# Kernel optimization log

Measured on AMD Instinct MI355X. Metric: run time of the kernel, lower is better.

The kernel has to match this reference:

```python
import jax, jax.numpy as jnp
import numpy as np

H = 768          # hidden_size
HH = H // 2      # 384


def setup_inputs() -> dict:
    key = jax.random.key(0)
    ks = jax.random.split(key, 16)
    B, W, E, R = 32, 512, 128, 1024
    inp = {
        "hidden_states": jax.random.normal(ks[0], (B, W, H), dtype=jnp.float32),
        "relation_head": jax.random.randint(ks[1], (B, R), 0, E),
        "relation_tail": jax.random.randint(ks[2], (B, R), 0, E),
        "relation_label": jax.random.randint(ks[3], (B, R), 0, 2),
        "entities_start": jax.random.randint(ks[4], (B, E), 0, W),
        "entities_end": jax.random.randint(ks[5], (B, E), 0, W),
        "entities_label": jax.random.randint(ks[6], (B, E), 0, 3),
        # parameters (torch Linear convention: weight [out, in])
        "entity_emb": jax.random.normal(ks[7], (3, H), dtype=jnp.float32) * 0.02,
        "Wh1": jax.random.normal(ks[8], (H, 2 * H), dtype=jnp.float32) * 0.02,
        "bh1": jnp.zeros((H,), jnp.float32),
        "Wh2": jax.random.normal(ks[9], (HH, H), dtype=jnp.float32) * 0.02,
        "bh2": jnp.zeros((HH,), jnp.float32),
        "Wt1": jax.random.normal(ks[10], (H, 2 * H), dtype=jnp.float32) * 0.02,
        "bt1": jnp.zeros((H,), jnp.float32),
        "Wt2": jax.random.normal(ks[11], (HH, H), dtype=jnp.float32) * 0.02,
        "bt2": jnp.zeros((HH,), jnp.float32),
        "W_bil": jax.random.normal(ks[12], (2, HH, HH), dtype=jnp.float32) * 0.02,
        "W_lin": jax.random.normal(ks[13], (2, 2 * HH), dtype=jnp.float32) * 0.02,
        "b_lin": jnp.zeros((2,), jnp.float32),
    }
    return inp


def _ffnn(x, W1, b1, W2, b2):
    # two-layer MLP with ReLU (dropout is identity in eval mode)
    h = jax.nn.relu(jnp.einsum('brd,hd->brh', x, W1) + b1)
    return jax.nn.relu(jnp.einsum('brh,oh->bro', h, W2) + b2)


def reference(hidden_states, relation_head, relation_tail, relation_label,
              entities_start, entities_end, entities_label,
              entity_emb, Wh1, bh1, Wh2, bh2, Wt1, bt1, Wt2, bt2,
              W_bil, W_lin, b_lin):
    # gather per-relation entity info: [B, R]
    head_index = jnp.take_along_axis(entities_start, relation_head, axis=1)
    head_label = jnp.take_along_axis(entities_label, relation_head, axis=1)
    tail_index = jnp.take_along_axis(entities_start, relation_tail, axis=1)
    tail_label = jnp.take_along_axis(entities_label, relation_tail, axis=1)

    # gather token reprs: [B, R, H]
    head_tok = jnp.take_along_axis(hidden_states, head_index[:, :, None], axis=1)
    tail_tok = jnp.take_along_axis(hidden_states, tail_index[:, :, None], axis=1)

    head_repr = jnp.concatenate([head_tok, entity_emb[head_label]], axis=-1)  # [B,R,2H]
    tail_repr = jnp.concatenate([tail_tok, entity_emb[tail_label]], axis=-1)

    heads = _ffnn(head_repr, Wh1, bh1, Wh2, bh2)  # [B,R,HH]
    tails = _ffnn(tail_repr, Wt1, bt1, Wt2, bt2)

    # biaffine: bilinear + linear on concat
    bil = jnp.einsum('bri,oij,brj->bro', heads, W_bil, tails)
    lin = jnp.einsum('brc,oc->bro', jnp.concatenate([heads, tails], axis=-1), W_lin) + b_lin
    logits = bil + lin  # [B, R, 2]

    # per-doc mean CE summed over docs
    logp = jax.nn.log_softmax(logits, axis=-1)
    nll = -jnp.take_along_axis(logp, relation_label[:, :, None], axis=-1)[..., 0]  # [B,R]
    loss = jnp.sum(jnp.mean(nll, axis=1))
    return loss
```

## Files before the change

kernel.cpp:

```cpp
#include <hip/hip_runtime.h>
#include <math.h>

typedef unsigned short u16;
typedef __bf16 bf16x8 __attribute__((ext_vector_type(8)));
typedef float f32x4 __attribute__((ext_vector_type(4)));

#define B_ 32
#define W_ 512
#define H_ 768
#define HH_ 384
#define E_ 128
#define R_ 1024
#define BE_ (B_*E_)
#define K1_ (2*H_)

__device__ __forceinline__ u16 f2bf(float f) {
  unsigned u = __float_as_uint(f);
  u = (u + 0x7fffu + ((u >> 16) & 1u)) >> 16;
  return (u16)u;
}
__device__ __forceinline__ float bf2f(u16 u) {
  return __uint_as_float(((unsigned)u) << 16);
}

__device__ __forceinline__ void gload_lds16(const void* g, void* l) {
  __builtin_amdgcn_global_load_lds(
      (__attribute__((address_space(1))) void*)(g),
      (__attribute__((address_space(3))) void*)(l), 16, 0, 0);
}

__device__ __forceinline__ void xcd_swizzle(int& bx, int& by) {
  const int nwg = gridDim.x * gridDim.y;
  int orig = blockIdx.y * gridDim.x + blockIdx.x;
  int q = nwg >> 3, r = nwg & 7;
  int xcd = orig & 7, idx = orig >> 3;
  int wgid = (xcd < r ? xcd * (q + 1) : r * (q + 1) + (xcd - r) * q) + idx;
  bx = wgid % gridDim.x;
  by = wgid / gridDim.x;
}

#define NBLK_W 2017
#define NBLK_P 1152
#define NBLK_X 4096

__global__ __launch_bounds__(256) void prep_all(
    const float* __restrict__ Wh1, const float* __restrict__ Wt1,
    const float* __restrict__ Wh2, const float* __restrict__ Wt2,
    const float* __restrict__ Wbil,
    const float* __restrict__ bh1, const float* __restrict__ bt1,
    const float* __restrict__ bh2, const float* __restrict__ bt2,
    const float* __restrict__ emb,
    const float* __restrict__ hs, const int* __restrict__ ent_start,
    u16* __restrict__ W1c, u16* __restrict__ W2c, u16* __restrict__ Wb,
    float* __restrict__ b2cat, float* __restrict__ P, u16* __restrict__ X)
{
  const int blk = blockIdx.x;
  const int tid = threadIdx.x;

  if (blk < NBLK_W) {
    const int i = blk * 256 + tid;
    const int SW1 = 294912;
    const int SW2 = SW1 + 147456;
    const int SWB = SW2 + 73728;
    const int SB2 = SWB + 192;
    if (i < SW1) {
      int row = i / 192, c = i % 192;
      const float4* src = (const float4*)((row < 768)
          ? (Wh1 + (size_t)row * K1_) : (Wt1 + (size_t)(row - 768) * K1_));
      float4 v = src[c];
      ushort4 o; o.x = f2bf(v.x); o.y = f2bf(v.y); o.z = f2bf(v.z); o.w = f2bf(v.w);
      ((ushort4*)W1c)[i] = o;
    } else if (i < SW2) {
      int j = i - SW1;
      float4 v = (j < 73728) ? ((const float4*)Wh2)[j]
                             : ((const float4*)Wt2)[j - 73728];
      ushort4 o; o.x = f2bf(v.x); o.y = f2bf(v.y); o.z = f2bf(v.z); o.w = f2bf(v.w);
      ((ushort4*)W2c)[j] = o;
    } else if (i < SWB) {
      int j = i - SW2;
      float4 v = ((const float4*)Wbil)[j];
      ushort4 o; o.x = f2bf(v.x); o.y = f2bf(v.y); o.z = f2bf(v.z); o.w = f2bf(v.w);
      ((ushort4*)Wb)[j] = o;
    } else if (i < SB2) {
      int j = i - SWB;
      ((float4*)b2cat)[j] = (j < 96) ? ((const float4*)bh2)[j]
                                     : ((const float4*)bt2)[j - 96];
    }
  } else if (blk < NBLK_W + NBLK_P) {
    const int w = (blk - NBLK_W) * 4 + (tid >> 6);
    const int lane = tid & 63;
    const int l = w / K1_;
    const int n = w - l * K1_;
    const float* wrow = (n < 768) ? (Wh1 + (size_t)n * K1_ + 768)
                                  : (Wt1 + (size_t)(n - 768) * K1_ + 768);
    const float  bb   = (n < 768) ? bh1[n] : bt1[n - 768];
    const float* ev = emb + (size_t)l * H_;
    float s = 0.f;
#pragma unroll
    for (int t = 0; t < 12; ++t) {
      int d = lane + 64 * t;
      s += ev[d] * wrow[d];
    }
#pragma unroll
    for (int off = 32; off; off >>= 1) s += __shfl_down(s, off);
    if (lane == 0) P[(size_t)l * K1_ + n] = s + bb;
  } else {
    const int be = blk - (NBLK_W + NBLK_P);
    if (tid < 192) {
      int b = be >> 7;
      int start = ent_start[be];
      const float4* s0 = (const float4*)(hs + ((size_t)b * W_ + start) * H_);
      float4 v = s0[tid];
      ushort4 o; o.x = f2bf(v.x); o.y = f2bf(v.y); o.z = f2bf(v.z); o.w = f2bf(v.w);
      ((ushort4*)(X + (size_t)be * H_))[tid] = o;
    }
  }
}

#define BM 128
#define BN 128
#define BKK 64

__global__ __launch_bounds__(256, 2) void gemm_bf16(
    const u16* __restrict__ A, int lda,
    const u16* __restrict__ Wt,
    const float* __restrict__ bias,
    u16* __restrict__ C, int ldc,
    int M, int N, int K, int do_relu, int half_n, int aoff,
    const float* __restrict__ rowBias,
    const int* __restrict__ rowLabel, int ldP)
{
  __shared__ char smem[2 * 32768];

  int bx, by;
  xcd_swizzle(bx, by);
  const int bn = bx * BN;
  const int bm = by * BM;

  const int tid  = threadIdx.x;
  const int wid  = tid >> 6;
  const int lane = tid & 63;
  const int wm = ((wid >> 1) & 1) * 64;
  const int wn = (wid & 1) * 64;

  const int a0 = (half_n && bn >= half_n) ? aoff : 0;

  const int srow = lane >> 3;
  const int sk8  = (lane & 7) ^ srow;
  const u16* gA = A  + (size_t)(bm + 32*wid + srow) * lda + a0 + 8*sk8;
  const u16* gB = Wt + (size_t)(bn + 32*wid + srow) * K  + 8*sk8;

  const int frow = lane & 15;
  const int fk8  = lane >> 4;

  f32x4 acc[4][4] = {};

  auto stage = [&](int buf, int k0) {
    char* As = smem + buf * 32768;
    char* Bs = As + 16384;
#pragma unroll
    for (int i = 0; i < 4; ++i) {
      gload_lds16(gA + k0 + (size_t)i * 8 * lda, As + (4*wid + i) * 1024);
      gload_lds16(gB + k0 + (size_t)i * 8 * K,   Bs + (4*wid + i) * 1024);
    }
  };

  const int nt = K / BKK;
  stage(0, 0);
  asm volatile("s_waitcnt vmcnt(0)" ::: "memory");
  __syncthreads();

  for (int t = 0; t < nt; ++t) {
    const int cur = t & 1;
    if (t + 1 < nt) stage(cur ^ 1, (t + 1) * BKK);

    char* As = smem + cur * 32768;
    char* Bs = As + 16384;
#pragma unroll
    for (int kh = 0; kh < 2; ++kh) {
      bf16x8 a[4], b[4];
#pragma unroll
      for (int m = 0; m < 4; ++m) {
        const int row  = wm + m*16 + frow;
        const int slot = (kh*4 + fk8) ^ (row & 7);
        a[m] = *(const bf16x8*)(As + row*128 + slot*16);
      }
#pragma unroll
      for (int n = 0; n < 4; ++n) {
        const int row  = wn + n*16 + frow;
        const int slot = (kh*4 + fk8) ^ (row & 7);
        b[n] = *(const bf16x8*)(Bs + row*128 + slot*16);
      }
#pragma unroll
      for (int m = 0; m < 4; ++m)
#pragma unroll
        for (int n = 0; n < 4; ++n)
          acc[m][n] = __builtin_amdgcn_mfma_f32_16x16x32_bf16(
              a[m], b[n], acc[m][n], 0, 0, 0);
    }

    if (t + 1 < nt) {
      asm volatile("s_waitcnt vmcnt(0)" ::: "memory");
      __syncthreads();
    }
  }

  int lbl[4][4];
  if (rowLabel) {
#pragma unroll
    for (int m = 0; m < 4; ++m)
#pragma unroll
      for (int r = 0; r < 4; ++r)
        lbl[m][r] = rowLabel[bm + wm + m*16 + fk8*4 + r];
  }

#pragma unroll
  for (int n = 0; n < 4; ++n) {
    const int col = bn + wn + n*16 + frow;
    const float bv = bias ? bias[col] : 0.f;
    float p0 = 0.f, p1 = 0.f, p2 = 0.f;
    if (rowLabel) {
      p0 = rowBias[col];
      p1 = rowBias[ldP + col];
      p2 = rowBias[2*ldP + col];
    }
#pragma unroll
    for (int m = 0; m < 4; ++m) {
#pragma unroll
      for (int r = 0; r < 4; ++r) {
        const int row = bm + wm + m*16 + fk8*4 + r;
        float v = acc[m][n][r] + bv;
        if (rowLabel) {
          int l = lbl[m][r];
          v += (l == 0) ? p0 : ((l == 1) ? p1 : p2);
        }
        if (do_relu) v = fmaxf(v, 0.f);
        C[(size_t)row * ldc + col] = f2bf(v);
      }
    }
  }
}

__global__ __launch_bounds__(256, 2) void gemm_S(
    const u16* __restrict__ Hcat, const u16* __restrict__ U,
    const float* __restrict__ linHT, const float* __restrict__ b_lin,
    float* __restrict__ S)
{
  __shared__ char smem[2 * 16384];

  int bx, by;
  xcd_swizzle(bx, by);
  const int z  = by >> 1;
  const int bm = (by & 1) * 64;
  const int bn = bx * 64;

  const int tid  = threadIdx.x;
  const int wid  = tid >> 6;
  const int lane = tid & 63;
  const int wm = ((wid >> 1) & 1) * 32;
  const int wn = (wid & 1) * 32;

  const int srow = lane >> 3;
  const int sk8  = (lane & 7) ^ srow;
  const u16* gA = Hcat + (size_t)z * 98304 + (size_t)(bm + 16*wid + srow) * 768 + 8*sk8;
  const u16* gB = U    + (size_t)z * 98304 + (size_t)(bn + 16*wid + srow) * 384 + 8*sk8;

  const int frow = lane & 15;
  const int fk8  = lane >> 4;

  f32x4 acc[2][2] = {};

  auto stage = [&](int buf, int k0) {
    char* As = smem + buf * 16384;
    char* Bs = As + 8192;
#pragma unroll
    for (int i = 0; i < 2; ++i) {
      gload_lds16(gA + k0 + (size_t)i * 8 * 768, As + (2*wid + i) * 1024);
      gload_lds16(gB + k0 + (size_t)i * 8 * 384, Bs + (2*wid + i) * 1024);
    }
  };

  const int nt = 384 / BKK;
  stage(0, 0);
  asm volatile("s_waitcnt vmcnt(0)" ::: "memory");
  __syncthreads();

  for (int t = 0; t < nt; ++t) {
    const int cur = t & 1;
    if (t + 1 < nt) stage(cur ^ 1, (t + 1) * BKK);

    char* As = smem + cur * 16384;
    char* Bs = As + 8192;
#pragma unroll
    for (int kh = 0; kh < 2; ++kh) {
      bf16x8 a[2], b[2];
#pragma unroll
      for (int m = 0; m < 2; ++m) {
        const int row  = wm + m*16 + frow;
        const int slot = (kh*4 + fk8) ^ (row & 7);
        a[m] = *(const bf16x8*)(As + row*128 + slot*16);
      }
#pragma unroll
      for (int n = 0; n < 2; ++n) {
        const int row  = wn + n*16 + frow;
        const int slot = (kh*4 + fk8) ^ (row & 7);
        b[n] = *(const bf16x8*)(Bs + row*128 + slot*16);
      }
#pragma unroll
      for (int m = 0; m < 2; ++m)
#pragma unroll
        for (int n = 0; n < 2; ++n)
          acc[m][n] = __builtin_amdgcn_mfma_f32_16x16x32_bf16(
              a[m], b[n], acc[m][n], 0, 0, 0);
    }

    if (t + 1 < nt) {
      asm volatile("s_waitcnt vmcnt(0)" ::: "memory");
      __syncthreads();
    }
  }

  const int o = frow & 1;
  const float blv = b_lin[o];
  float linH[2][4];
#pragma unroll
  for (int m = 0; m < 2; ++m)
#pragma unroll
    for (int r = 0; r < 4; ++r)
      linH[m][r] = linHT[(size_t)(z*128 + bm + wm + m*16 + fk8*4 + r) * 4 + o];

#pragma unroll
  for (int n = 0; n < 2; ++n) {
    const int n_out = bn + wn + n*16 + frow;
    const int e2 = n_out >> 1;
    const float lt = linHT[(size_t)(z*128 + e2) * 4 + 2 + o];
#pragma unroll
    for (int m = 0; m < 2; ++m) {
#pragma unroll
      for (int r = 0; r < 4; ++r) {
        const int row = bm + wm + m*16 + fk8*4 + r;
        S[((size_t)(z*128 + row)) * 256 + n_out] =
            acc[m][n][r] + linH[m][r] + lt + blv;
      }
    }
  }
}

__global__ __launch_bounds__(256) void lin_parts_kernel(
    const u16* __restrict__ Hcat, const float* __restrict__ W_lin,
    float* __restrict__ linHT, float* __restrict__ out)
{
  if (blockIdx.x == 0 && threadIdx.x == 0) out[0] = 0.f;
  const int wave = blockIdx.x * 4 + (threadIdx.x >> 6);
  const int lane = threadIdx.x & 63;
  const int nwave = gridDim.x * 4;

  for (int be = wave; be < BE_; be += nwave) {
    const ushort4* src = (const ushort4*)(Hcat + (size_t)be * 768);
    float s0 = 0.f, s1 = 0.f, s2 = 0.f, s3 = 0.f;
#pragma unroll
    for (int rd = 0; rd < 3; ++rd) {
      const int idx4 = rd * 64 + lane;
      const int c = idx4 * 4;
      ushort4 v4 = src[idx4];
      float4 w0 = *(const float4*)(W_lin + c);
      float4 w1 = *(const float4*)(W_lin + 768 + c);
      float d0 = bf2f(v4.x)*w0.x + bf2f(v4.y)*w0.y + bf2f(v4.z)*w0.z + bf2f(v4.w)*w0.w;
      float d1 = bf2f(v4.x)*w1.x + bf2f(v4.y)*w1.y + bf2f(v4.z)*w1.z + bf2f(v4.w)*w1.w;
      if (c < 384) { s0 += d0; s1 += d1; }
      else         { s2 += d0; s3 += d1; }
    }
#pragma unroll
    for (int off = 32; off; off >>= 1) {
      s0 += __shfl_down(s0, off);
      s1 += __shfl_down(s1, off);
      s2 += __shfl_down(s2, off);
      s3 += __shfl_down(s3, off);
    }
    if (lane == 0) {
      float4 v = {s0, s1, s2, s3};
      *(float4*)(linHT + (size_t)be * 4) = v;
    }
  }
}

__global__ __launch_bounds__(256) void ce_kernel(
    const int* __restrict__ rel_head, const int* __restrict__ rel_tail,
    const int* __restrict__ rel_label, const float* __restrict__ S,
    float* __restrict__ out)
{
  const int i = blockIdx.x * 256 + threadIdx.x;
  const int b  = i >> 10;
  const int rh = rel_head[i];
  const int rt = rel_tail[i];
  const int lab = rel_label[i];
  const float2 lv = *(const float2*)(S + ((size_t)(b*E_ + rh)) * 256 + rt*2);
  const float l0 = lv.x, l1 = lv.y;
  const float m = fmaxf(l0, l1);
  const float lse = m + logf(expf(l0 - m) + expf(l1 - m));
  float nll = lse - (lab == 0 ? l0 : l1);

#pragma unroll
  for (int off = 32; off; off >>= 1) nll += __shfl_down(nll, off);
  __shared__ float red[4];
  if ((threadIdx.x & 63) == 0) red[threadIdx.x >> 6] = nll;
  __syncthreads();
  if (threadIdx.x == 0)
    atomicAdd(out, (red[0] + red[1] + red[2] + red[3]) * (1.0f / R_));
}

extern "C" void kernel_launch(void* const* d_in, const int* in_sizes, int n_in,
                              void* d_out, int out_size, void* d_ws, size_t ws_size,
                              hipStream_t stream)
{
  const float* hs        = (const float*)d_in[0];
  const int*   rel_head  = (const int*)  d_in[1];
  const int*   rel_tail  = (const int*)  d_in[2];
  const int*   rel_label = (const int*)  d_in[3];
  const int*   ent_start = (const int*)  d_in[4];
  const int*   ent_label = (const int*)  d_in[6];
  const float* emb   = (const float*)d_in[7];
  const float* Wh1   = (const float*)d_in[8];
  const float* bh1   = (const float*)d_in[9];
  const float* Wh2   = (const float*)d_in[10];
  const float* bh2   = (const float*)d_in[11];
  const float* Wt1   = (const float*)d_in[12];
  const float* bt1   = (const float*)d_in[13];
  const float* Wt2   = (const float*)d_in[14];
  const float* bt2   = (const float*)d_in[15];
  const float* W_bil = (const float*)d_in[16];
  const float* W_lin = (const float*)d_in[17];
  const float* b_lin = (const float*)d_in[18];
  float* out = (float*)d_out;

  u16* X    = (u16*)d_ws;
  u16* H1   = X    + (size_t)BE_ * H_;
  u16* Hcat = H1   + (size_t)BE_ * K1_;
  u16* U    = Hcat + (size_t)BE_ * H_;
  u16* W1c  = U    + (size_t)BE_ * H_;
  u16* W2c  = W1c  + (size_t)K1_ * H_;
  u16* Wb   = W2c  + (size_t)H_ * H_;
  float* b2cat = (float*)(Wb + (size_t)H_ * HH_);
  float* P     = b2cat + H_;
  float* linHT = P + 3*K1_;
  float* S     = linHT + 4*BE_;

  prep_all<<<dim3(NBLK_W + NBLK_P + NBLK_X), dim3(256), 0, stream>>>(
      Wh1, Wt1, Wh2, Wt2, W_bil, bh1, bt1, bh2, bt2, emb,
      hs, ent_start, W1c, W2c, Wb, b2cat, P, X);

  gemm_bf16<<<dim3(K1_/BN, BE_/BM), dim3(256), 0, stream>>>(
      X, H_, W1c, (const float*)nullptr, H1, K1_, BE_, K1_, H_, 1, 0, 0,
      P, ent_label, K1_);

  gemm_bf16<<<dim3(H_/BN, BE_/BM), dim3(256), 0, stream>>>(
      H1, K1_, W2c, b2cat, Hcat, H_, BE_, H_, H_, 1, HH_, H_,
      (const float*)nullptr, (const int*)nullptr, 0);

  lin_parts_kernel<<<dim3(128), dim3(256), 0, stream>>>(Hcat, W_lin, linHT, out);

  gemm_bf16<<<dim3(H_/BN, BE_/BM), dim3(256), 0, stream>>>(
      Hcat + HH_, H_, Wb, (const float*)nullptr, U, H_, BE_, H_, HH_, 0, 0, 0,
      (const float*)nullptr, (const int*)nullptr, 0);

  gemm_S<<<dim3(4, 2*B_), dim3(256), 0, stream>>>(Hcat, U, linHT, b_lin, S);

  ce_kernel<<<dim3(B_*R_/256), dim3(256), 0, stream>>>(
      rel_head, rel_tail, rel_label, S, out);
}
```

Measured before the change: 68.35 us.

## Shrink GEMM tiles, fuse lin-parts into U GEMM, fuse CE into S GEMM

```diff
diff --git a/kernel.cpp b/kernel.cpp
--- a/kernel.cpp
+++ b/kernel.cpp
@@ -13,6 +13,7 @@
 #define R_ 1024
 #define BE_ (B_*E_)
 #define K1_ (2*H_)
+#define BKK 64
 
 __device__ __forceinline__ u16 f2bf(float f) {
   unsigned u = __float_as_uint(f);
@@ -27,16 +28,6 @@
   __builtin_amdgcn_global_load_lds(
       (__attribute__((address_space(1))) void*)(g),
       (__attribute__((address_space(3))) void*)(l), 16, 0, 0);
-}
-
-__device__ __forceinline__ void xcd_swizzle(int& bx, int& by) {
-  const int nwg = gridDim.x * gridDim.y;
-  int orig = blockIdx.y * gridDim.x + blockIdx.x;
-  int q = nwg >> 3, r = nwg & 7;
-  int xcd = orig & 7, idx = orig >> 3;
-  int wgid = (xcd < r ? xcd * (q + 1) : r * (q + 1) + (xcd - r) * q) + idx;
-  bx = wgid % gridDim.x;
-  by = wgid / gridDim.x;
 }
 
 #define NBLK_W 2017
@@ -117,53 +108,97 @@
   }
 }
 
-#define BM 128
-#define BN 128
-#define BKK 64
-
-__global__ __launch_bounds__(256, 2) void gemm_bf16(
+template<int TBM, int TBN, int MINB>
+__global__ __launch_bounds__(256, MINB) void gemm_t(
     const u16* __restrict__ A, int lda,
     const u16* __restrict__ Wt,
     const float* __restrict__ bias,
-    u16* __restrict__ C, int ldc,
-    int M, int N, int K, int do_relu, int half_n, int aoff,
+    u16* __restrict__ C, int ldc, int K,
+    int do_relu, int half_n, int aoff,
     const float* __restrict__ rowBias,
-    const int* __restrict__ rowLabel, int ldP)
+    const int* __restrict__ rowLabel, int ldP,
+    int nbx, int ngemm,
+    const u16* __restrict__ linSrc, const float* __restrict__ W_lin,
+    float* __restrict__ linHT, float* __restrict__ out)
 {
-  __shared__ char smem[2 * 32768];
-
-  int bx, by;
-  xcd_swizzle(bx, by);
-  const int bn = bx * BN;
-  const int bm = by * BM;
+  constexpr int FM = TBM / 32;
+  constexpr int FN = TBN / 32;
+  constexpr int UNITS = (TBM + TBN) / 8;
+  constexpr int UPW = UNITS / 4;
+  constexpr int BUFB = (TBM + TBN) * 128;
+
+  __shared__ char smem[2 * BUFB];
 
   const int tid  = threadIdx.x;
   const int wid  = tid >> 6;
   const int lane = tid & 63;
-  const int wm = ((wid >> 1) & 1) * 64;
-  const int wn = (wid & 1) * 64;
+
+  if ((int)blockIdx.x >= ngemm) {
+    if ((int)blockIdx.x == ngemm && tid == 0) out[0] = 0.f;
+    const int nblk  = gridDim.x - ngemm;
+    const int wave  = ((int)blockIdx.x - ngemm) * 4 + wid;
+    const int nwave = nblk * 4;
+    for (int be = wave; be < BE_; be += nwave) {
+      const ushort4* src = (const ushort4*)(linSrc + (size_t)be * 768);
+      float s0 = 0.f, s1 = 0.f, s2 = 0.f, s3 = 0.f;
+#pragma unroll
+      for (int rd = 0; rd < 3; ++rd) {
+        const int idx4 = rd * 64 + lane;
+        const int c = idx4 * 4;
+        ushort4 v4 = src[idx4];
+        float4 w0 = *(const float4*)(W_lin + c);
+        float4 w1 = *(const float4*)(W_lin + 768 + c);
+        float d0 = bf2f(v4.x)*w0.x + bf2f(v4.y)*w0.y + bf2f(v4.z)*w0.z + bf2f(v4.w)*w0.w;
+        float d1 = bf2f(v4.x)*w1.x + bf2f(v4.y)*w1.y + bf2f(v4.z)*w1.z + bf2f(v4.w)*w1.w;
+        if (c < 384) { s0 += d0; s1 += d1; }
+        else         { s2 += d0; s3 += d1; }
+      }
+#pragma unroll
+      for (int off = 32; off; off >>= 1) {
+        s0 += __shfl_down(s0, off);
+        s1 += __shfl_down(s1, off);
+        s2 += __shfl_down(s2, off);
+        s3 += __shfl_down(s3, off);
+      }
+      if (lane == 0) {
+        float4 v = {s0, s1, s2, s3};
+        *(float4*)(linHT + (size_t)be * 4) = v;
+      }
+    }
+    return;
+  }
+
+  const int q = ngemm >> 3, r = ngemm & 7;
+  const int xcd = blockIdx.x & 7, idx = blockIdx.x >> 3;
+  const int wgid = (xcd < r ? xcd * (q + 1) : r * (q + 1) + (xcd - r) * q) + idx;
+  const int bn = (wgid % nbx) * TBN;
+  const int bm = (wgid / nbx) * TBM;
 
   const int a0 = (half_n && bn >= half_n) ? aoff : 0;
-
   const int srow = lane >> 3;
   const int sk8  = (lane & 7) ^ srow;
-  const u16* gA = A  + (size_t)(bm + 32*wid + srow) * lda + a0 + 8*sk8;
-  const u16* gB = Wt + (size_t)(bn + 32*wid + srow) * K  + 8*sk8;
-
+
+  auto stage = [&](int buf, int k0) {
+    char* base = smem + buf * BUFB;
+#pragma unroll
+    for (int i = 0; i < UPW; ++i) {
+      const int u = wid * UPW + i;
+      if (u < TBM / 8) {
+        const int row = bm + u * 8 + srow;
+        gload_lds16(A + (size_t)row * lda + a0 + k0 + 8 * sk8, base + u * 1024);
+      } else {
+        const int row = bn + (u - TBM / 8) * 8 + srow;
+        gload_lds16(Wt + (size_t)row * K + k0 + 8 * sk8, base + u * 1024);
+      }
+    }
+  };
+
+  const int wm = (wid >> 1) * (TBM / 2);
+  const int wn = (wid & 1) * (TBN / 2);
   const int frow = lane & 15;
   const int fk8  = lane >> 4;
 
-  f32x4 acc[4][4] = {};
-
-  auto stage = [&](int buf, int k0) {
-    char* As = smem + buf * 32768;
-    char* Bs = As + 16384;
-#pragma unroll
-    for (int i = 0; i < 4; ++i) {
-      gload_lds16(gA + k0 + (size_t)i * 8 * lda, As + (4*wid + i) * 1024);
-      gload_lds16(gB + k0 + (size_t)i * 8 * K,   Bs + (4*wid + i) * 1024);
-    }
-  };
+  f32x4 acc[FM][FN] = {};
 
   const int nt = K / BKK;
   stage(0, 0);
@@ -174,27 +209,27 @@
     const int cur = t & 1;
     if (t + 1 < nt) stage(cur ^ 1, (t + 1) * BKK);
 
-    char* As = smem + cur * 32768;
-    char* Bs = As + 16384;
+    char* As = smem + cur * BUFB;
+    char* Bs = As + TBM * 128;
 #pragma unroll
     for (int kh = 0; kh < 2; ++kh) {
-      bf16x8 a[4], b[4];
-#pragma unroll
-      for (int m = 0; m < 4; ++m) {
+      bf16x8 a[FM], b[FN];
+#pragma unroll
+      for (int m = 0; m < FM; ++m) {
         const int row  = wm + m*16 + frow;
         const int slot = (kh*4 + fk8) ^ (row & 7);
         a[m] = *(const bf16x8*)(As + row*128 + slot*16);
       }
 #pragma unroll
-      for (int n = 0; n < 4; ++n) {
+      for (int n = 0; n < FN; ++n) {
         const int row  = wn + n*16 + frow;
         const int slot = (kh*4 + fk8) ^ (row & 7);
         b[n] = *(const bf16x8*)(Bs + row*128 + slot*16);
       }
 #pragma unroll
-      for (int m = 0; m < 4; ++m)
-#pragma unroll
-        for (int n = 0; n < 4; ++n)
+      for (int m = 0; m < FM; ++m)
+#pragma unroll
+        for (int n = 0; n < FN; ++n)
           acc[m][n] = __builtin_amdgcn_mfma_f32_16x16x32_bf16(
               a[m], b[n], acc[m][n], 0, 0, 0);
     }
@@ -205,17 +240,17 @@
     }
   }
 
-  int lbl[4][4];
+  int lbl[FM][4];
   if (rowLabel) {
 #pragma unroll
-    for (int m = 0; m < 4; ++m)
+    for (int m = 0; m < FM; ++m)
 #pragma unroll
       for (int r = 0; r < 4; ++r)
         lbl[m][r] = rowLabel[bm + wm + m*16 + fk8*4 + r];
   }
 
 #pragma unroll
-  for (int n = 0; n < 4; ++n) {
+  for (int n = 0; n < FN; ++n) {
     const int col = bn + wn + n*16 + frow;
     const float bv = bias ? bias[col] : 0.f;
     float p0 = 0.f, p1 = 0.f, p2 = 0.f;
@@ -225,7 +260,7 @@
       p2 = rowBias[2*ldP + col];
     }
 #pragma unroll
-    for (int m = 0; m < 4; ++m) {
+    for (int m = 0; m < FM; ++m) {
 #pragma unroll
       for (int r = 0; r < 4; ++r) {
         const int row = bm + wm + m*16 + fk8*4 + r;
@@ -241,53 +276,59 @@
   }
 }
 
-__global__ __launch_bounds__(256, 2) void gemm_S(
+__global__ __launch_bounds__(256, 2) void gemm_S_ce(
     const u16* __restrict__ Hcat, const u16* __restrict__ U,
     const float* __restrict__ linHT, const float* __restrict__ b_lin,
-    float* __restrict__ S)
+    const int* __restrict__ rel_head, const int* __restrict__ rel_tail,
+    const int* __restrict__ rel_label, float* __restrict__ out)
 {
   __shared__ char smem[2 * 16384];
-
-  int bx, by;
-  xcd_swizzle(bx, by);
-  const int z  = by >> 1;
-  const int bm = (by & 1) * 64;
-  const int bn = bx * 64;
+  __shared__ float Sl[64][65];
+  __shared__ float red[4];
+
+  const int xcd = blockIdx.x & 7, idx = blockIdx.x >> 3;
+  const int wgid = xcd * 32 + idx;
+  const int bn = (wgid & 3) * 64;
+  const int zz = wgid >> 2;
+  const int z  = zz >> 1;
+  const int bm = (zz & 1) * 64;
 
   const int tid  = threadIdx.x;
   const int wid  = tid >> 6;
   const int lane = tid & 63;
-  const int wm = ((wid >> 1) & 1) * 32;
-  const int wn = (wid & 1) * 32;
-
   const int srow = lane >> 3;
   const int sk8  = (lane & 7) ^ srow;
-  const u16* gA = Hcat + (size_t)z * 98304 + (size_t)(bm + 16*wid + srow) * 768 + 8*sk8;
-  const u16* gB = U    + (size_t)z * 98304 + (size_t)(bn + 16*wid + srow) * 384 + 8*sk8;
-
+
+  auto stage = [&](int buf, int k0) {
+    char* base = smem + buf * 16384;
+#pragma unroll
+    for (int i = 0; i < 4; ++i) {
+      const int u = wid * 4 + i;
+      if (u < 8) {
+        const int row = z*128 + bm + u*8 + srow;
+        gload_lds16(Hcat + (size_t)row * 768 + k0 + 8*sk8, base + u*1024);
+      } else {
+        const int row = bn + (u - 8)*8 + srow;
+        gload_lds16(U + (size_t)z*98304 + (size_t)row * 384 + k0 + 8*sk8,
+                    base + u*1024);
+      }
+    }
+  };
+
+  const int wm = (wid >> 1) * 32;
+  const int wn = (wid & 1) * 32;
   const int frow = lane & 15;
   const int fk8  = lane >> 4;
 
   f32x4 acc[2][2] = {};
 
-  auto stage = [&](int buf, int k0) {
-    char* As = smem + buf * 16384;
-    char* Bs = As + 8192;
-#pragma unroll
-    for (int i = 0; i < 2; ++i) {
-      gload_lds16(gA + k0 + (size_t)i * 8 * 768, As + (2*wid + i) * 1024);
-      gload_lds16(gB + k0 + (size_t)i * 8 * 384, Bs + (2*wid + i) * 1024);
-    }
-  };
-
-  const int nt = 384 / BKK;
   stage(0, 0);
   asm volatile("s_waitcnt vmcnt(0)" ::: "memory");
   __syncthreads();
 
-  for (int t = 0; t < nt; ++t) {
+  for (int t = 0; t < 6; ++t) {
     const int cur = t & 1;
-    if (t + 1 < nt) stage(cur ^ 1, (t + 1) * BKK);
+    if (t + 1 < 6) stage(cur ^ 1, (t + 1) * BKK);
 
     char* As = smem + cur * 16384;
     char* Bs = As + 8192;
@@ -314,98 +355,52 @@
               a[m], b[n], acc[m][n], 0, 0, 0);
     }
 
-    if (t + 1 < nt) {
+    if (t + 1 < 6) {
       asm volatile("s_waitcnt vmcnt(0)" ::: "memory");
       __syncthreads();
     }
   }
+  __syncthreads();
 
   const int o = frow & 1;
   const float blv = b_lin[o];
-  float linH[2][4];
-#pragma unroll
-  for (int m = 0; m < 2; ++m)
-#pragma unroll
-    for (int r = 0; r < 4; ++r)
-      linH[m][r] = linHT[(size_t)(z*128 + bm + wm + m*16 + fk8*4 + r) * 4 + o];
-
 #pragma unroll
   for (int n = 0; n < 2; ++n) {
-    const int n_out = bn + wn + n*16 + frow;
-    const int e2 = n_out >> 1;
+    const int lc = wn + n*16 + frow;
+    const int e2 = (bn + lc) >> 1;
     const float lt = linHT[(size_t)(z*128 + e2) * 4 + 2 + o];
 #pragma unroll
     for (int m = 0; m < 2; ++m) {
 #pragma unroll
       for (int r = 0; r < 4; ++r) {
-        const int row = bm + wm + m*16 + fk8*4 + r;
-        S[((size_t)(z*128 + row)) * 256 + n_out] =
-            acc[m][n][r] + linH[m][r] + lt + blv;
-      }
-    }
-  }
-}
-
-__global__ __launch_bounds__(256) void lin_parts_kernel(
-    const u16* __restrict__ Hcat, const float* __restrict__ W_lin,
-    float* __restrict__ linHT, float* __restrict__ out)
-{
-  if (blockIdx.x == 0 && threadIdx.x == 0) out[0] = 0.f;
-  const int wave = blockIdx.x * 4 + (threadIdx.x >> 6);
-  const int lane = threadIdx.x & 63;
-  const int nwave = gridDim.x * 4;
-
-  for (int be = wave; be < BE_; be += nwave) {
-    const ushort4* src = (const ushort4*)(Hcat + (size_t)be * 768);
-    float s0 = 0.f, s1 = 0.f, s2 = 0.f, s3 = 0.f;
-#pragma unroll
-    for (int rd = 0; rd < 3; ++rd) {
-      const int idx4 = rd * 64 + lane;
-      const int c = idx4 * 4;
-      ushort4 v4 = src[idx4];
-      float4 w0 = *(const float4*)(W_lin + c);
-      float4 w1 = *(const float4*)(W_lin + 768 + c);
-      float d0 = bf2f(v4.x)*w0.x + bf2f(v4.y)*w0.y + bf2f(v4.z)*w0.z + bf2f(v4.w)*w0.w;
-      float d1 = bf2f(v4.x)*w1.x + bf2f(v4.y)*w1.y + bf2f(v4.z)*w1.z + bf2f(v4.w)*w1.w;
-      if (c < 384) { s0 += d0; s1 += d1; }
-      else         { s2 += d0; s3 += d1; }
-    }
-#pragma unroll
-    for (int off = 32; off; off >>= 1) {
-      s0 += __shfl_down(s0, off);
-      s1 += __shfl_down(s1, off);
-      s2 += __shfl_down(s2, off);
-      s3 += __shfl_down(s3, off);
-    }
-    if (lane == 0) {
-      float4 v = {s0, s1, s2, s3};
-      *(float4*)(linHT + (size_t)be * 4) = v;
-    }
-  }
-}
-
-__global__ __launch_bounds__(256) void ce_kernel(
-    const int* __restrict__ rel_head, const int* __restrict__ rel_tail,
-    const int* __restrict__ rel_label, const float* __restrict__ S,
-    float* __restrict__ out)
-{
-  const int i = blockIdx.x * 256 + threadIdx.x;
-  const int b  = i >> 10;
-  const int rh = rel_head[i];
-  const int rt = rel_tail[i];
-  const int lab = rel_label[i];
-  const float2 lv = *(const float2*)(S + ((size_t)(b*E_ + rh)) * 256 + rt*2);
-  const float l0 = lv.x, l1 = lv.y;
-  const float m = fmaxf(l0, l1);
-  const float lse = m + logf(expf(l0 - m) + expf(l1 - m));
-  float nll = lse - (lab == 0 ? l0 : l1);
-
-#pragma unroll
-  for (int off = 32; off; off >>= 1) nll += __shfl_down(nll, off);
-  __shared__ float red[4];
-  if ((threadIdx.x & 63) == 0) red[threadIdx.x >> 6] = nll;
+        const int lr = wm + m*16 + fk8*4 + r;
+        const float lh = linHT[(size_t)(z*128 + bm + lr) * 4 + o];
+        Sl[lr][lc] = acc[m][n][r] + lh + lt + blv;
+      }
+    }
+  }
   __syncthreads();
-  if (threadIdx.x == 0)
+
+  float nllsum = 0.f;
+#pragma unroll
+  for (int j = 0; j < 4; ++j) {
+    const int i = z * 1024 + tid + 256 * j;
+    const int rh = rel_head[i];
+    const int rt = rel_tail[i];
+    const int lab = rel_label[i];
+    if ((unsigned)(rh - bm) < 64u && (unsigned)(rt*2 - bn) < 64u) {
+      const float l0 = Sl[rh - bm][rt*2 - bn];
+      const float l1 = Sl[rh - bm][rt*2 - bn + 1];
+      const float mx = fmaxf(l0, l1);
+      const float lse = mx + logf(expf(l0 - mx) + expf(l1 - mx));
+      nllsum += lse - (lab == 0 ? l0 : l1);
+    }
+  }
+#pragma unroll
+  for (int off = 32; off; off >>= 1) nllsum += __shfl_down(nllsum, off);
+  if (lane == 0) red[wid] = nllsum;
+  __syncthreads();
+  if (tid == 0)
     atomicAdd(out, (red[0] + red[1] + red[2] + red[3]) * (1.0f / R_));
 }
 
@@ -443,28 +438,26 @@
   float* b2cat = (float*)(Wb + (size_t)H_ * HH_);
   float* P     = b2cat + H_;
   float* linHT = P + 3*K1_;
-  float* S     = linHT + 4*BE_;
 
   prep_all<<<dim3(NBLK_W + NBLK_P + NBLK_X), dim3(256), 0, stream>>>(
       Wh1, Wt1, Wh2, Wt2, W_bil, bh1, bt1, bh2, bt2, emb,
       hs, ent_start, W1c, W2c, Wb, b2cat, P, X);
 
-  gemm_bf16<<<dim3(K1_/BN, BE_/BM), dim3(256), 0, stream>>>(
-      X, H_, W1c, (const float*)nullptr, H1, K1_, BE_, K1_, H_, 1, 0, 0,
-      P, ent_label, K1_);
-
-  gemm_bf16<<<dim3(H_/BN, BE_/BM), dim3(256), 0, stream>>>(
-      H1, K1_, W2c, b2cat, Hcat, H_, BE_, H_, H_, 1, HH_, H_,
-      (const float*)nullptr, (const int*)nullptr, 0);
-
-  lin_parts_kernel<<<dim3(128), dim3(256), 0, stream>>>(Hcat, W_lin, linHT, out);
-
-  gemm_bf16<<<dim3(H_/BN, BE_/BM), dim3(256), 0, stream>>>(
-      Hcat + HH_, H_, Wb, (const float*)nullptr, U, H_, BE_, H_, HH_, 0, 0, 0,
-      (const float*)nullptr, (const int*)nullptr, 0);
-
-  gemm_S<<<dim3(4, 2*B_), dim3(256), 0, stream>>>(Hcat, U, linHT, b_lin, S);
-
-  ce_kernel<<<dim3(B_*R_/256), dim3(256), 0, stream>>>(
-      rel_head, rel_tail, rel_label, S, out);
-}
+  gemm_t<64,128,3><<<dim3(768), dim3(256), 0, stream>>>(
+      X, H_, W1c, (const float*)nullptr, H1, K1_, H_, 1, 0, 0,
+      P, ent_label, K1_, 12, 768,
+      (const u16*)nullptr, (const float*)nullptr, (float*)nullptr, (float*)nullptr);
+
+  gemm_t<64,64,4><<<dim3(768), dim3(256), 0, stream>>>(
+      H1, K1_, W2c, b2cat, Hcat, H_, H_, 1, HH_, H_,
+      (const float*)nullptr, (const int*)nullptr, 0, 12, 768,
+      (const u16*)nullptr, (const float*)nullptr, (float*)nullptr, (float*)nullptr);
+
+  gemm_t<64,64,4><<<dim3(768 + 16), dim3(256), 0, stream>>>(
+      Hcat + HH_, H_, Wb, (const float*)nullptr, U, H_, HH_, 0, 0, 0,
+      (const float*)nullptr, (const int*)nullptr, 0, 12, 768,
+      Hcat, W_lin, linHT, out);
+
+  gemm_S_ce<<<dim3(256), dim3(256), 0, stream>>>(
+      Hcat, U, linHT, b_lin, rel_head, rel_tail, rel_label, out);
+}
```

After: 96.60 us. 1.41x slower.

## Fuse score GEMM with cross-entropy and relax GEMM pipeline waits

Applied to the files above, without the earlier changes.

```diff
diff --git a/kernel.cpp b/kernel.cpp
--- a/kernel.cpp
+++ b/kernel.cpp
@@ -13,6 +13,7 @@
 #define R_ 1024
 #define BE_ (B_*E_)
 #define K1_ (2*H_)
+#define BKK 64
 
 __device__ __forceinline__ u16 f2bf(float f) {
   unsigned u = __float_as_uint(f);
@@ -119,7 +120,6 @@
 
 #define BM 128
 #define BN 128
-#define BKK 64
 
 __global__ __launch_bounds__(256, 2) void gemm_bf16(
     const u16* __restrict__ A, int lda,
@@ -167,12 +167,16 @@
 
   const int nt = K / BKK;
   stage(0, 0);
-  asm volatile("s_waitcnt vmcnt(0)" ::: "memory");
-  __syncthreads();
 
   for (int t = 0; t < nt; ++t) {
     const int cur = t & 1;
-    if (t + 1 < nt) stage(cur ^ 1, (t + 1) * BKK);
+    if (t + 1 < nt) {
+      stage(cur ^ 1, (t + 1) * BKK);
+      asm volatile("s_waitcnt vmcnt(8)" ::: "memory");
+    } else {
+      asm volatile("s_waitcnt vmcnt(0)" ::: "memory");
+    }
+    __syncthreads();
 
     char* As = smem + cur * 32768;
     char* Bs = As + 16384;
@@ -199,10 +203,8 @@
               a[m], b[n], acc[m][n], 0, 0, 0);
     }
 
-    if (t + 1 < nt) {
-      asm volatile("s_waitcnt vmcnt(0)" ::: "memory");
+    if (t + 1 < nt)
       __syncthreads();
-    }
   }
 
   int lbl[4][4];
@@ -241,53 +243,63 @@
   }
 }
 
-__global__ __launch_bounds__(256, 2) void gemm_S(
+__global__ __launch_bounds__(256, 2) void gemm_S_ce(
     const u16* __restrict__ Hcat, const u16* __restrict__ U,
     const float* __restrict__ linHT, const float* __restrict__ b_lin,
-    float* __restrict__ S)
+    const int* __restrict__ rel_head, const int* __restrict__ rel_tail,
+    const int* __restrict__ rel_label, float* __restrict__ out)
 {
   __shared__ char smem[2 * 16384];
-
-  int bx, by;
-  xcd_swizzle(bx, by);
-  const int z  = by >> 1;
-  const int bm = (by & 1) * 64;
-  const int bn = bx * 64;
+  __shared__ float Sl[64][65];
+  __shared__ float red[4];
+
+  const int xcd = blockIdx.x & 7, idx = blockIdx.x >> 3;
+  const int wgid = xcd * 32 + idx;
+  const int bn = (wgid & 3) * 64;
+  const int zz = wgid >> 2;
+  const int z  = zz >> 1;
+  const int bm = (zz & 1) * 64;
 
   const int tid  = threadIdx.x;
   const int wid  = tid >> 6;
   const int lane = tid & 63;
-  const int wm = ((wid >> 1) & 1) * 32;
-  const int wn = (wid & 1) * 32;
-
   const int srow = lane >> 3;
   const int sk8  = (lane & 7) ^ srow;
-  const u16* gA = Hcat + (size_t)z * 98304 + (size_t)(bm + 16*wid + srow) * 768 + 8*sk8;
-  const u16* gB = U    + (size_t)z * 98304 + (size_t)(bn + 16*wid + srow) * 384 + 8*sk8;
-
+
+  auto stage = [&](int buf, int k0) {
+    char* base = smem + buf * 16384;
+#pragma unroll
+    for (int i = 0; i < 4; ++i) {
+      const int u = wid * 4 + i;
+      if (u < 8) {
+        const int row = z*128 + bm + u*8 + srow;
+        gload_lds16(Hcat + (size_t)row * 768 + k0 + 8*sk8, base + u*1024);
+      } else {
+        const int row = bn + (u - 8)*8 + srow;
+        gload_lds16(U + (size_t)z*98304 + (size_t)row * 384 + k0 + 8*sk8,
+                    base + u*1024);
+      }
+    }
+  };
+
+  const int wm = (wid >> 1) * 32;
+  const int wn = (wid & 1) * 32;
   const int frow = lane & 15;
   const int fk8  = lane >> 4;
 
   f32x4 acc[2][2] = {};
 
-  auto stage = [&](int buf, int k0) {
-    char* As = smem + buf * 16384;
-    char* Bs = As + 8192;
-#pragma unroll
-    for (int i = 0; i < 2; ++i) {
-      gload_lds16(gA + k0 + (size_t)i * 8 * 768, As + (2*wid + i) * 1024);
-      gload_lds16(gB + k0 + (size_t)i * 8 * 384, Bs + (2*wid + i) * 1024);
-    }
-  };
-
-  const int nt = 384 / BKK;
   stage(0, 0);
-  asm volatile("s_waitcnt vmcnt(0)" ::: "memory");
-  __syncthreads();
-
-  for (int t = 0; t < nt; ++t) {
+
+  for (int t = 0; t < 6; ++t) {
     const int cur = t & 1;
-    if (t + 1 < nt) stage(cur ^ 1, (t + 1) * BKK);
+    if (t + 1 < 6) {
+      stage(cur ^ 1, (t + 1) * BKK);
+      asm volatile("s_waitcnt vmcnt(4)" ::: "memory");
+    } else {
+      asm volatile("s_waitcnt vmcnt(0)" ::: "memory");
+    }
+    __syncthreads();
 
     char* As = smem + cur * 16384;
     char* Bs = As + 8192;
@@ -314,36 +326,50 @@
               a[m], b[n], acc[m][n], 0, 0, 0);
     }
 
-    if (t + 1 < nt) {
-      asm volatile("s_waitcnt vmcnt(0)" ::: "memory");
+    if (t + 1 < 6)
       __syncthreads();
-    }
   }
 
   const int o = frow & 1;
   const float blv = b_lin[o];
-  float linH[2][4];
-#pragma unroll
-  for (int m = 0; m < 2; ++m)
-#pragma unroll
-    for (int r = 0; r < 4; ++r)
-      linH[m][r] = linHT[(size_t)(z*128 + bm + wm + m*16 + fk8*4 + r) * 4 + o];
-
 #pragma unroll
   for (int n = 0; n < 2; ++n) {
-    const int n_out = bn + wn + n*16 + frow;
-    const int e2 = n_out >> 1;
+    const int lc = wn + n*16 + frow;
+    const int e2 = (bn + lc) >> 1;
     const float lt = linHT[(size_t)(z*128 + e2) * 4 + 2 + o];
 #pragma unroll
     for (int m = 0; m < 2; ++m) {
 #pragma unroll
       for (int r = 0; r < 4; ++r) {
-        const int row = bm + wm + m*16 + fk8*4 + r;
-        S[((size_t)(z*128 + row)) * 256 + n_out] =
-            acc[m][n][r] + linH[m][r] + lt + blv;
-      }
-    }
-  }
+        const int lr = wm + m*16 + fk8*4 + r;
+        const float lh = linHT[(size_t)(z*128 + bm + lr) * 4 + o];
+        Sl[lr][lc] = acc[m][n][r] + lh + lt + blv;
+      }
+    }
+  }
+  __syncthreads();
+
+  float nllsum = 0.f;
+#pragma unroll
+  for (int j = 0; j < 4; ++j) {
+    const int i = z * 1024 + tid + 256 * j;
+    const int rh = rel_head[i];
+    const int rt = rel_tail[i];
+    const int lab = rel_label[i];
+    if ((unsigned)(rh - bm) < 64u && (unsigned)(rt*2 - bn) < 64u) {
+      const float l0 = Sl[rh - bm][rt*2 - bn];
+      const float l1 = Sl[rh - bm][rt*2 - bn + 1];
+      const float mx = fmaxf(l0, l1);
+      const float lse = mx + logf(expf(l0 - mx) + expf(l1 - mx));
+      nllsum += lse - (lab == 0 ? l0 : l1);
+    }
+  }
+#pragma unroll
+  for (int off = 32; off; off >>= 1) nllsum += __shfl_down(nllsum, off);
+  if (lane == 0) red[wid] = nllsum;
+  __syncthreads();
+  if (tid == 0)
+    atomicAdd(out, (red[0] + red[1] + red[2] + red[3]) * (1.0f / R_));
 }
 
 __global__ __launch_bounds__(256) void lin_parts_kernel(
@@ -382,31 +408,6 @@
       *(float4*)(linHT + (size_t)be * 4) = v;
     }
   }
-}
-
-__global__ __launch_bounds__(256) void ce_kernel(
-    const int* __restrict__ rel_head, const int* __restrict__ rel_tail,
-    const int* __restrict__ rel_label, const float* __restrict__ S,
-    float* __restrict__ out)
-{
-  const int i = blockIdx.x * 256 + threadIdx.x;
-  const int b  = i >> 10;
-  const int rh = rel_head[i];
-  const int rt = rel_tail[i];
-  const int lab = rel_label[i];
-  const float2 lv = *(const float2*)(S + ((size_t)(b*E_ + rh)) * 256 + rt*2);
-  const float l0 = lv.x, l1 = lv.y;
-  const float m = fmaxf(l0, l1);
-  const float lse = m + logf(expf(l0 - m) + expf(l1 - m));
-  float nll = lse - (lab == 0 ? l0 : l1);
-
-#pragma unroll
-  for (int off = 32; off; off >>= 1) nll += __shfl_down(nll, off);
-  __shared__ float red[4];
-  if ((threadIdx.x & 63) == 0) red[threadIdx.x >> 6] = nll;
-  __syncthreads();
-  if (threadIdx.x == 0)
-    atomicAdd(out, (red[0] + red[1] + red[2] + red[3]) * (1.0f / R_));
 }
 
 extern "C" void kernel_launch(void* const* d_in, const int* in_sizes, int n_in,
@@ -443,7 +444,6 @@
   float* b2cat = (float*)(Wb + (size_t)H_ * HH_);
   float* P     = b2cat + H_;
   float* linHT = P + 3*K1_;
-  float* S     = linHT + 4*BE_;
 
   prep_all<<<dim3(NBLK_W + NBLK_P + NBLK_X), dim3(256), 0, stream>>>(
       Wh1, Wt1, Wh2, Wt2, W_bil, bh1, bt1, bh2, bt2, emb,
@@ -463,8 +463,6 @@
       Hcat + HH_, H_, Wb, (const float*)nullptr, U, H_, BE_, H_, HH_, 0, 0, 0,
       (const float*)nullptr, (const int*)nullptr, 0);
 
-  gemm_S<<<dim3(4, 2*B_), dim3(256), 0, stream>>>(Hcat, U, linHT, b_lin, S);
-
-  ce_kernel<<<dim3(B_*R_/256), dim3(256), 0, stream>>>(
-      rel_head, rel_tail, rel_label, S, out);
-}
+  gemm_S_ce<<<dim3(256), dim3(256), 0, stream>>>(
+      Hcat, U, linHT, b_lin, rel_head, rel_tail, rel_label, out);
+}
```

Result: slower. 76.60 us (+12.1%).
